# Kernel optimization log

Measured on AMD Instinct MI355X. Metric: run time of the kernel, lower is better.

## Reference

```python
import jax, jax.numpy as jnp
import numpy as np

H = 16   # n_heads == n_I
D = 64   # d_q = d_k = d_v = d_r
DX = H * D
B, S = 4, 2048

def setup_inputs() -> dict:
    key = jax.random.key(0)
    ks = jax.random.split(key, 9)
    sc = 0.02
    return {
        "value": jax.random.normal(ks[0], (B, S, DX), jnp.float32),
        "key":   jax.random.normal(ks[1], (B, S, DX), jnp.float32),
        "query": jax.random.normal(ks[2], (B, S, DX), jnp.float32),
        "Wq_w": jax.random.normal(ks[3], (DX, DX), jnp.float32) * sc,
        "Wq_b": jnp.zeros((DX,), jnp.float32),
        "Wk_w": jax.random.normal(ks[4], (DX, DX), jnp.float32) * sc,
        "Wk_b": jnp.zeros((DX,), jnp.float32),
        "Wv_w": jax.random.normal(ks[5], (DX, DX), jnp.float32) * sc,
        "Wv_b": jnp.zeros((DX,), jnp.float32),
        "Wr_w": jax.random.normal(ks[6], (DX, DX), jnp.float32) * sc,
        "Wr_b": jnp.zeros((DX,), jnp.float32),
        "Wout_w": jax.random.normal(ks[7], (DX, DX), jnp.float32) * sc,
        "Wout_b": jnp.zeros((DX,), jnp.float32),
    }

def _heads(x, b, s):
    # [b, s, H*D] -> [b, H, s, D]
    return x.reshape(b, s, H, D).transpose(0, 2, 1, 3)

def reference(value, key, query, Wq_w, Wq_b, Wk_w, Wk_b, Wv_w, Wv_b,
              Wr_w, Wr_b, Wout_w, Wout_b):
    b, s, _ = query.shape
    # torch nn.Linear: y = x @ W.T + b
    Q = _heads(query @ Wq_w.T + Wq_b, b, s)   # [b,H,s,D]
    K = _heads(key   @ Wk_w.T + Wk_b, b, s)
    V = _heads(value @ Wv_w.T + Wv_b, b, s)
    R = _heads(query @ Wr_w.T + Wr_b, b, s)
    dot_scale = jnp.sqrt(jnp.float32(D))
    scores = jnp.einsum("bhid,bhjd->bhij", Q, K) / dot_scale  # [b,H,s,s]
    attn = jax.nn.softmax(scores, axis=-1)                    # dropout p=0
    out = jnp.einsum("bhij,bhjd->bhid", attn, V)              # [b,H,s,D]
    out = out * R                                             # R-gating
    out = out.transpose(0, 2, 1, 3).reshape(b, s, H * D)
    return out @ Wout_w.T + Wout_b
```

## Files before the change

### kernel.cpp

```cpp
#include <hip/hip_runtime.h>
#include <hip/hip_bf16.h>

typedef __bf16 bf16;
typedef __bf16 bf16x4 __attribute__((ext_vector_type(4)));
typedef __bf16 bf16x8 __attribute__((ext_vector_type(8)));
typedef float  f32x4  __attribute__((ext_vector_type(4)));

#define MFMA_16x16x32(a, b, c) __builtin_amdgcn_mfma_f32_16x16x32_bf16((a), (b), (c), 0, 0, 0)

typedef const void __attribute__((address_space(1))) gvoid;
typedef void __attribute__((address_space(3))) svoid;

__device__ __forceinline__ void async_copy16(const void* gptr, void* ldsptr) {
    __builtin_amdgcn_global_load_lds((gvoid*)gptr, (svoid*)ldsptr, 16, 0, 0);
}

__device__ __forceinline__ int swz8(int row, int quad) {
    return (quad ^ ((row >> 1) & 3)) * 8;
}

__device__ __forceinline__ unsigned cvt_pk_bf16(float a, float b) {
    unsigned r;
    asm("v_cvt_pk_bf16_f32 %0, %1, %2" : "=v"(r) : "v"(a), "v"(b));
    return r;
}

__global__ void cvt3_acts(const float* __restrict__ s0, const float* __restrict__ s1,
                          const float* __restrict__ s2,
                          bf16* __restrict__ d0, bf16* __restrict__ d1, bf16* __restrict__ d2)
{
    constexpr int N4SEG = 8192 * 1024 / 4;
    int i = blockIdx.x * blockDim.x + threadIdx.x;
    const int stride = gridDim.x * blockDim.x;
    for (; i < 3 * N4SEG; i += stride) {
        const int seg = i / N4SEG;
        const int j = i - seg * N4SEG;
        const float* s = seg == 0 ? s0 : (seg == 1 ? s1 : s2);
        bf16* d = seg == 0 ? d0 : (seg == 1 ? d1 : d2);
        float4 v = ((const float4*)s)[j];
        bf16x4 o = { (bf16)v.x, (bf16)v.y, (bf16)v.z, (bf16)v.w };
        ((bf16x4*)d)[j] = o;
    }
}

__global__ void cvt5_wts(const float* __restrict__ s0, const float* __restrict__ s1,
                         const float* __restrict__ s2, const float* __restrict__ s3,
                         const float* __restrict__ s4,
                         bf16* __restrict__ d0, bf16* __restrict__ d1, bf16* __restrict__ d2,
                         bf16* __restrict__ d3, bf16* __restrict__ d4)
{
    constexpr int N4SEG = 1024 * 1024 / 4;
    int i = blockIdx.x * blockDim.x + threadIdx.x;
    const int stride = gridDim.x * blockDim.x;
    for (; i < 5 * N4SEG; i += stride) {
        const int seg = i / N4SEG;
        const int j = i - seg * N4SEG;
        const float* s = seg == 0 ? s0 : seg == 1 ? s1 : seg == 2 ? s2 : seg == 3 ? s3 : s4;
        bf16* d = seg == 0 ? d0 : seg == 1 ? d1 : seg == 2 ? d2 : seg == 3 ? d3 : d4;
        float4 v = ((const float4*)s)[j];
        bf16x4 o = { (bf16)v.x, (bf16)v.y, (bf16)v.z, (bf16)v.w };
        ((bf16x4*)d)[j] = o;
    }
}

__global__ void proj_fused(const bf16* __restrict__ xq, const bf16* __restrict__ xk,
                           const bf16* __restrict__ xv, const bf16* __restrict__ wall,
                           const float* __restrict__ ball,
                           bf16* __restrict__ qr, bf16* __restrict__ kws,
                           bf16* __restrict__ vtws)
{
    constexpr int K = 1024, SDIM = 2048;
    __shared__ alignas(16) bf16 As[2][128 * 32];
    __shared__ alignas(16) bf16 Bs[2][128 * 32];

    const int tid  = threadIdx.x;
    const int lane = tid & 63;
    const int wave = tid >> 6;
    const int wm   = wave >> 1;
    const int wn   = wave & 1;
    const int bm   = blockIdx.x * 128;
    const int by   = blockIdx.y;
    const int bn   = by * 128;
    const int l15  = lane & 15;
    const int quad = lane >> 4;

    const bf16* X = (by < 16) ? xq : (by < 24 ? xk : xv);

    const int srow = lane >> 2;
    const int scol = (lane & 3) * 8;

    const bf16* aseg0 = X + (size_t)(bm + wave * 32 + srow) * K + scol;
    const bf16* aseg1 = X + (size_t)(bm + wave * 32 + 16 + srow) * K + scol;
    const bf16* bseg0 = wall + (size_t)(bn + wave * 32 + srow) * K + scol;
    const bf16* bseg1 = wall + (size_t)(bn + wave * 32 + 16 + srow) * K + scol;

    f32x4 acc[4][4] = {};

    async_copy16(aseg0, As[0] + (wave * 2 + 0) * 512);
    async_copy16(aseg1, As[0] + (wave * 2 + 1) * 512);
    async_copy16(bseg0, Bs[0] + (wave * 2 + 0) * 512);
    async_copy16(bseg1, Bs[0] + (wave * 2 + 1) * 512);

    for (int k0 = 0; k0 < K; k0 += 32) {
        const int cur = (k0 >> 5) & 1;
        __syncthreads();
        if (k0 + 32 < K) {
            const int nxt = cur ^ 1;
            async_copy16(aseg0 + k0 + 32, As[nxt] + (wave * 2 + 0) * 512);
            async_copy16(aseg1 + k0 + 32, As[nxt] + (wave * 2 + 1) * 512);
            async_copy16(bseg0 + k0 + 32, Bs[nxt] + (wave * 2 + 0) * 512);
            async_copy16(bseg1 + k0 + 32, Bs[nxt] + (wave * 2 + 1) * 512);
        }

        bf16x8 af[4], bfr[4];
        #pragma unroll
        for (int i = 0; i < 4; ++i)
            af[i] = *(const bf16x8*)(As[cur] + (wm * 64 + i * 16 + l15) * 32 + quad * 8);
        #pragma unroll
        for (int j = 0; j < 4; ++j)
            bfr[j] = *(const bf16x8*)(Bs[cur] + (wn * 64 + j * 16 + l15) * 32 + quad * 8);
        #pragma unroll
        for (int i = 0; i < 4; ++i)
            #pragma unroll
            for (int j = 0; j < 4; ++j)
                acc[i][j] = MFMA_16x16x32(af[i], bfr[j], acc[i][j]);
    }

    #pragma unroll
    for (int i = 0; i < 4; ++i) {
        const int rowg = bm + wm * 64 + i * 16 + quad * 4;
        #pragma unroll
        for (int j = 0; j < 4; ++j) {
            const int colg = bn + wn * 64 + j * 16 + l15;
            const float bv = ball[colg];
            if (by < 16) {
                #pragma unroll
                for (int r = 0; r < 4; ++r)
                    qr[(size_t)(rowg + r) * 2048 + colg] = (bf16)(acc[i][j][r] + bv);
            } else if (by < 24) {
                const int cl = colg - 2048;
                #pragma unroll
                for (int r = 0; r < 4; ++r)
                    kws[(size_t)(rowg + r) * 1024 + cl] = (bf16)(acc[i][j][r] + bv);
            } else {
                const int d = colg - 3072;
                bf16x4 o;
                #pragma unroll
                for (int r = 0; r < 4; ++r) o[r] = (bf16)(acc[i][j][r] + bv);
                *(bf16x4*)(vtws + (size_t)(rowg >> 11) * 1024 * SDIM
                                + (size_t)d * SDIM + (rowg & (SDIM - 1))) = o;
            }
        }
    }
}

__global__ void gemm_out(const bf16* __restrict__ X, const bf16* __restrict__ W,
                         const float* __restrict__ bias, float* __restrict__ Y)
{
    constexpr int K = 1024, N = 1024;
    __shared__ alignas(16) bf16 As[2][128 * 32];
    __shared__ alignas(16) bf16 Bs[2][128 * 32];

    const int tid  = threadIdx.x;
    const int lane = tid & 63;
    const int wave = tid >> 6;
    const int wm   = wave >> 1;
    const int wn   = wave & 1;
    const int bm   = blockIdx.x * 128;
    const int bn   = blockIdx.y * 128;
    const int l15  = lane & 15;
    const int quad = lane >> 4;

    const int srow = lane >> 2;
    const int scol = (lane & 3) * 8;

    const bf16* aseg0 = X + (size_t)(bm + wave * 32 + srow) * K + scol;
    const bf16* aseg1 = X + (size_t)(bm + wave * 32 + 16 + srow) * K + scol;
    const bf16* bseg0 = W + (size_t)(bn + wave * 32 + srow) * K + scol;
    const bf16* bseg1 = W + (size_t)(bn + wave * 32 + 16 + srow) * K + scol;

    f32x4 acc[4][4] = {};

    async_copy16(aseg0, As[0] + (wave * 2 + 0) * 512);
    async_copy16(aseg1, As[0] + (wave * 2 + 1) * 512);
    async_copy16(bseg0, Bs[0] + (wave * 2 + 0) * 512);
    async_copy16(bseg1, Bs[0] + (wave * 2 + 1) * 512);

    for (int k0 = 0; k0 < K; k0 += 32) {
        const int cur = (k0 >> 5) & 1;
        __syncthreads();
        if (k0 + 32 < K) {
            const int nxt = cur ^ 1;
            async_copy16(aseg0 + k0 + 32, As[nxt] + (wave * 2 + 0) * 512);
            async_copy16(aseg1 + k0 + 32, As[nxt] + (wave * 2 + 1) * 512);
            async_copy16(bseg0 + k0 + 32, Bs[nxt] + (wave * 2 + 0) * 512);
            async_copy16(bseg1 + k0 + 32, Bs[nxt] + (wave * 2 + 1) * 512);
        }

        bf16x8 af[4], bfr[4];
        #pragma unroll
        for (int i = 0; i < 4; ++i)
            af[i] = *(const bf16x8*)(As[cur] + (wm * 64 + i * 16 + l15) * 32 + quad * 8);
        #pragma unroll
        for (int j = 0; j < 4; ++j)
            bfr[j] = *(const bf16x8*)(Bs[cur] + (wn * 64 + j * 16 + l15) * 32 + quad * 8);
        #pragma unroll
        for (int i = 0; i < 4; ++i)
            #pragma unroll
            for (int j = 0; j < 4; ++j)
                acc[i][j] = MFMA_16x16x32(af[i], bfr[j], acc[i][j]);
    }

    #pragma unroll
    for (int i = 0; i < 4; ++i) {
        const int rowg = bm + wm * 64 + i * 16 + quad * 4;
        #pragma unroll
        for (int j = 0; j < 4; ++j) {
            const int colg = bn + wn * 64 + j * 16 + l15;
            const float bv = bias[colg];
            #pragma unroll
            for (int r = 0; r < 4; ++r)
                Y[(size_t)(rowg + r) * N + colg] = acc[i][j][r] + bv;
        }
    }
}

__launch_bounds__(256, 2)
__global__ void attn_fused(const bf16* __restrict__ QRp, const bf16* __restrict__ Kp,
                           const bf16* __restrict__ Vtp, bf16* __restrict__ Op)
{
    constexpr int S = 2048, DXc = 1024, QRST = 2048, Dh = 64;
    constexpr int PST = 40;
    constexpr int NT = S / 64;
    __shared__ alignas(16) bf16 Ks[2][2][64 * 32];
    __shared__ alignas(16) bf16 Pt[4][2][2][16 * PST];

    const int tid  = threadIdx.x;
    const int lane = tid & 63;
    const int wave = tid >> 6;
    const int qt = blockIdx.x, h = blockIdx.y, b = blockIdx.z;
    const int l15  = lane & 15;
    const int quad = lane >> 4;

    const size_t qrbase = ((size_t)b * S) * QRST + h * Dh;
    const size_t kbase  = ((size_t)b * S) * DXc + h * Dh;
    const size_t vtbase = ((size_t)(b * 16 + h) * Dh) * S;
    const size_t obase  = ((size_t)b * S) * DXc + h * Dh;

    const int srow = lane >> 2;
    const int scol = ((lane & 3) ^ ((srow >> 1) & 3)) * 8;
    const bf16* kseg = Kp + kbase + (size_t)(16 * wave + srow) * DXc + scol;
    const int soff = wave * 512;

    const bf16* vwp = Vtp + vtbase + (size_t)l15 * S + quad * 8;

    async_copy16(kseg,      &Ks[0][0][soff]);
    async_copy16(kseg + 32, &Ks[0][1][soff]);

    constexpr float QSCALE = 0.125f * 1.44269504088896340736f;
    bf16x8 qf[2][2];
    #pragma unroll
    for (int mi = 0; mi < 2; ++mi) {
        const int qrow = qt * 128 + wave * 32 + mi * 16 + l15;
        const bf16* qptr = QRp + qrbase + (size_t)qrow * QRST + quad * 8;
        qf[mi][0] = *(const bf16x8*)(qptr);
        qf[mi][1] = *(const bf16x8*)(qptr + 32);
        #pragma unroll
        for (int j = 0; j < 8; ++j) {
            qf[mi][0][j] = (bf16)((float)qf[mi][0][j] * QSCALE);
            qf[mi][1][j] = (bf16)((float)qf[mi][1][j] * QSCALE);
        }
    }

    bf16x8 onef;
    #pragma unroll
    for (int j = 0; j < 8; ++j) onef[j] = (bf16)1.0f;

    f32x4 oacc[2][4] = {};
    f32x4 lsacc[2] = {};

    for (int t = 0; t < NT; ++t) {
        const int cur = t & 1;
        const int kv0 = t * 64;
        __syncthreads();
        if (t + 1 < NT) {
            const int nxt = cur ^ 1;
            const size_t ko = (size_t)(t + 1) * 64 * DXc;
            async_copy16(kseg + ko,      &Ks[nxt][0][soff]);
            async_copy16(kseg + ko + 32, &Ks[nxt][1][soff]);
        }

        bf16x8 vtf[2][4];
        #pragma unroll
        for (int half = 0; half < 2; ++half)
            #pragma unroll
            for (int db = 0; db < 4; ++db)
                vtf[half][db] = *(const bf16x8*)(vwp + (size_t)(db * 16) * S
                                                 + kv0 + half * 32);

        f32x4 st[2][4];
        #pragma unroll
        for (int nb = 0; nb < 4; ++nb) {
            bf16x8 kf0 = *(const bf16x8*)(&Ks[cur][0][0] + (nb * 16 + l15) * 32 + swz8(l15, quad));
            bf16x8 kf1 = *(const bf16x8*)(&Ks[cur][1][0] + (nb * 16 + l15) * 32 + swz8(l15, quad));
            #pragma unroll
            for (int mi = 0; mi < 2; ++mi) {
                f32x4 z = {0.f, 0.f, 0.f, 0.f};
                z = MFMA_16x16x32(kf1, qf[mi][1], z);
                st[mi][nb] = MFMA_16x16x32(kf0, qf[mi][0], z);
            }
        }
        #pragma unroll
        for (int mi = 0; mi < 2; ++mi) {
            #pragma unroll
            for (int nb = 0; nb < 4; ++nb) {
                const float p0 = __builtin_exp2f(st[mi][nb][0]);
                const float p1 = __builtin_exp2f(st[mi][nb][1]);
                const float p2 = __builtin_exp2f(st[mi][nb][2]);
                const float p3 = __builtin_exp2f(st[mi][nb][3]);
                uint2 w;
                w.x = cvt_pk_bf16(p0, p1);
                w.y = cvt_pk_bf16(p2, p3);
                *(uint2*)(&Pt[wave][mi][nb >> 1][0] + l15 * PST
                          + (nb & 1) * 16 + quad * 4) = w;
            }
        }
        #pragma unroll
        for (int half = 0; half < 2; ++half) {
            #pragma unroll
            for (int mi = 0; mi < 2; ++mi) {
                bf16x8 pf = *(const bf16x8*)(&Pt[wave][mi][half][0]
                                             + l15 * PST + quad * 8);
                #pragma unroll
                for (int db = 0; db < 4; ++db)
                    oacc[mi][db] = MFMA_16x16x32(vtf[half][db], pf, oacc[mi][db]);
                lsacc[mi] = MFMA_16x16x32(onef, pf, lsacc[mi]);
            }
        }
    }

    #pragma unroll
    for (int mi = 0; mi < 2; ++mi) {
        const float inv = 1.0f / lsacc[mi][0];
        const int qrow = qt * 128 + wave * 32 + mi * 16 + l15;
        const bf16* rrow = QRp + qrbase + (size_t)qrow * QRST + 1024;
        bf16* orow = Op + obase + (size_t)qrow * DXc;
        #pragma unroll
        for (int db = 0; db < 4; ++db) {
            bf16x4 rg = *(const bf16x4*)(rrow + db * 16 + quad * 4);
            bf16x4 o;
            #pragma unroll
            for (int r = 0; r < 4; ++r)
                o[r] = (bf16)(oacc[mi][db][r] * inv * (float)rg[r]);
            *(bf16x4*)(orow + db * 16 + quad * 4) = o;
        }
    }
}

extern "C" void kernel_launch(void* const* d_in, const int* in_sizes, int n_in,
                              void* d_out, int out_size, void* d_ws, size_t ws_size,
                              hipStream_t stream)
{
    (void)in_sizes; (void)n_in; (void)out_size; (void)ws_size;
    constexpr int B = 4, S = 2048, DX = 1024, M = B * S;
    constexpr size_t MD = (size_t)M * DX;
    constexpr size_t WD = (size_t)DX * DX;

    const float* value  = (const float*)d_in[0];
    const float* keyi   = (const float*)d_in[1];
    const float* query  = (const float*)d_in[2];
    const float* Wq_w   = (const float*)d_in[3];
    const float* Wq_b   = (const float*)d_in[4];
    const float* Wk_w   = (const float*)d_in[5];
    const float* Wk_b   = (const float*)d_in[6];
    const float* Wv_w   = (const float*)d_in[7];
    const float* Wv_b   = (const float*)d_in[8];
    const float* Wr_w   = (const float*)d_in[9];
    const float* Wr_b   = (const float*)d_in[10];
    const float* Wout_w = (const float*)d_in[11];
    const float* Wout_b = (const float*)d_in[12];

    bf16* p = (bf16*)d_ws;
    bf16* xv   = p;  p += MD;
    bf16* xk   = p;  p += MD;
    bf16* xq   = p;  p += MD;
    bf16* wall = p;  p += 4 * WD;
    bf16* wo   = p;  p += WD;
    bf16* qr   = p;  p += 2 * MD;
    bf16* kws  = p;  p += MD;
    bf16* vtws = p;  p += MD;
    float* ball = (float*)p;
    bf16* ows = xv;

    hipMemcpyAsync(ball,            Wq_b, DX * sizeof(float), hipMemcpyDeviceToDevice, stream);
    hipMemcpyAsync(ball + DX,       Wr_b, DX * sizeof(float), hipMemcpyDeviceToDevice, stream);
    hipMemcpyAsync(ball + 2 * DX,   Wk_b, DX * sizeof(float), hipMemcpyDeviceToDevice, stream);
    hipMemcpyAsync(ball + 3 * DX,   Wv_b, DX * sizeof(float), hipMemcpyDeviceToDevice, stream);

    cvt3_acts<<<dim3(2048), dim3(256), 0, stream>>>(value, keyi, query, xv, xk, xq);
    cvt5_wts <<<dim3(1024), dim3(256), 0, stream>>>(Wq_w, Wr_w, Wk_w, Wv_w, Wout_w,
                                                    wall, wall + WD, wall + 2 * WD,
                                                    wall + 3 * WD, wo);

    proj_fused<<<dim3(M / 128, 32), dim3(256), 0, stream>>>(
        xq, xk, xv, wall, ball, qr, kws, vtws);

    attn_fused<<<dim3(S / 128, 16, B), dim3(256), 0, stream>>>(qr, kws, vtws, ows);

    gemm_out<<<dim3(M / 128, DX / 128), dim3(256), 0, stream>>>(
        ows, wo, Wout_b, (float*)d_out);
}
```

Before: 480.5 us.

## Stage V tiles in LDS, remap GEMM workgroups, fold bias copies into weight conversion

The attention kernel now loads both K and V^T tiles into LDS through async copies each iteration, replacing V fragment loads straight from global memory. The K/V double buffering is dropped in favour of two barriers per tile. Occupancy is raised to 4 blocks per CU, and the grid is reordered so heads vary fastest. Both GEMMs get an XCD-aware workgroup remapping to improve L2 locality, and the four bias memcpys are folded into the weight-conversion kernel to save launches. Losing the prefetch overlap could expose K/V load latency, which the added occupancy is meant to hide.

```diff
diff --git a/kernel.cpp b/kernel.cpp
--- a/kernel.cpp
+++ b/kernel.cpp
@@ -46,12 +46,20 @@
 __global__ void cvt5_wts(const float* __restrict__ s0, const float* __restrict__ s1,
                          const float* __restrict__ s2, const float* __restrict__ s3,
                          const float* __restrict__ s4,
+                         const float* __restrict__ bq, const float* __restrict__ br,
+                         const float* __restrict__ bk, const float* __restrict__ bv,
                          bf16* __restrict__ d0, bf16* __restrict__ d1, bf16* __restrict__ d2,
-                         bf16* __restrict__ d3, bf16* __restrict__ d4)
+                         bf16* __restrict__ d3, bf16* __restrict__ d4,
+                         float* __restrict__ ball)
 {
     constexpr int N4SEG = 1024 * 1024 / 4;
     int i = blockIdx.x * blockDim.x + threadIdx.x;
     const int stride = gridDim.x * blockDim.x;
+    if (i < 4096) {
+        const int seg = i >> 10, j = i & 1023;
+        const float* b = seg == 0 ? bq : seg == 1 ? br : seg == 2 ? bk : bv;
+        ball[i] = b[j];
+    }
     for (; i < 5 * N4SEG; i += stride) {
         const int seg = i / N4SEG;
         const int j = i - seg * N4SEG;
@@ -73,13 +81,17 @@
     __shared__ alignas(16) bf16 As[2][128 * 32];
     __shared__ alignas(16) bf16 Bs[2][128 * 32];
 
+    const int lin  = blockIdx.x + 64 * blockIdx.y;
+    const int wgid = (lin & 7) * 256 + (lin >> 3);
+    const int bxr  = wgid & 63;
+    const int by   = wgid >> 6;
+
     const int tid  = threadIdx.x;
     const int lane = tid & 63;
     const int wave = tid >> 6;
     const int wm   = wave >> 1;
     const int wn   = wave & 1;
-    const int bm   = blockIdx.x * 128;
-    const int by   = blockIdx.y;
+    const int bm   = bxr * 128;
     const int bn   = by * 128;
     const int l15  = lane & 15;
     const int quad = lane >> 4;
@@ -161,13 +173,18 @@
     __shared__ alignas(16) bf16 As[2][128 * 32];
     __shared__ alignas(16) bf16 Bs[2][128 * 32];
 
+    const int lin  = blockIdx.x + 64 * blockIdx.y;
+    const int wgid = (lin & 7) * 64 + (lin >> 3);
+    const int bxr  = wgid & 63;
+    const int byr  = wgid >> 6;
+
     const int tid  = threadIdx.x;
     const int lane = tid & 63;
     const int wave = tid >> 6;
     const int wm   = wave >> 1;
     const int wn   = wave & 1;
-    const int bm   = blockIdx.x * 128;
-    const int bn   = blockIdx.y * 128;
+    const int bm   = bxr * 128;
+    const int bn   = byr * 128;
     const int l15  = lane & 15;
     const int quad = lane >> 4;
 
@@ -225,20 +242,20 @@
     }
 }
 
-__launch_bounds__(256, 2)
+__launch_bounds__(256, 4)
 __global__ void attn_fused(const bf16* __restrict__ QRp, const bf16* __restrict__ Kp,
                            const bf16* __restrict__ Vtp, bf16* __restrict__ Op)
 {
     constexpr int S = 2048, DXc = 1024, QRST = 2048, Dh = 64;
     constexpr int PST = 40;
-    constexpr int NT = S / 64;
-    __shared__ alignas(16) bf16 Ks[2][2][64 * 32];
+    __shared__ alignas(16) bf16 KsLo[64 * 32], KsHi[64 * 32];
+    __shared__ alignas(16) bf16 VtLo[64 * 32], VtHi[64 * 32];
     __shared__ alignas(16) bf16 Pt[4][2][2][16 * PST];
 
     const int tid  = threadIdx.x;
     const int lane = tid & 63;
     const int wave = tid >> 6;
-    const int qt = blockIdx.x, h = blockIdx.y, b = blockIdx.z;
+    const int h = blockIdx.x, qt = blockIdx.y, b = blockIdx.z;
     const int l15  = lane & 15;
     const int quad = lane >> 4;
 
@@ -246,16 +263,6 @@
     const size_t kbase  = ((size_t)b * S) * DXc + h * Dh;
     const size_t vtbase = ((size_t)(b * 16 + h) * Dh) * S;
     const size_t obase  = ((size_t)b * S) * DXc + h * Dh;
-
-    const int srow = lane >> 2;
-    const int scol = ((lane & 3) ^ ((srow >> 1) & 3)) * 8;
-    const bf16* kseg = Kp + kbase + (size_t)(16 * wave + srow) * DXc + scol;
-    const int soff = wave * 512;
-
-    const bf16* vwp = Vtp + vtbase + (size_t)l15 * S + quad * 8;
-
-    async_copy16(kseg,      &Ks[0][0][soff]);
-    async_copy16(kseg + 32, &Ks[0][1][soff]);
 
     constexpr float QSCALE = 0.125f * 1.44269504088896340736f;
     bf16x8 qf[2][2];
@@ -279,30 +286,28 @@
     f32x4 oacc[2][4] = {};
     f32x4 lsacc[2] = {};
 
-    for (int t = 0; t < NT; ++t) {
-        const int cur = t & 1;
-        const int kv0 = t * 64;
+    const int srow = lane >> 2;
+    const int scol = ((lane & 3) ^ ((srow >> 1) & 3)) * 8;
+    const bf16* kseg = Kp  + kbase  + (size_t)(16 * wave + srow) * DXc + scol;
+    const bf16* vseg = Vtp + vtbase + (size_t)(16 * wave + srow) * S   + scol;
+    bf16* ksl = KsLo + wave * 512;
+    bf16* ksh = KsHi + wave * 512;
+    bf16* vtl = VtLo + wave * 512;
+    bf16* vth = VtHi + wave * 512;
+
+    for (int kv0 = 0; kv0 < S; kv0 += 64) {
         __syncthreads();
-        if (t + 1 < NT) {
-            const int nxt = cur ^ 1;
-            const size_t ko = (size_t)(t + 1) * 64 * DXc;
-            async_copy16(kseg + ko,      &Ks[nxt][0][soff]);
-            async_copy16(kseg + ko + 32, &Ks[nxt][1][soff]);
-        }
-
-        bf16x8 vtf[2][4];
-        #pragma unroll
-        for (int half = 0; half < 2; ++half)
-            #pragma unroll
-            for (int db = 0; db < 4; ++db)
-                vtf[half][db] = *(const bf16x8*)(vwp + (size_t)(db * 16) * S
-                                                 + kv0 + half * 32);
+        async_copy16(kseg + (size_t)kv0 * DXc,      ksl);
+        async_copy16(kseg + (size_t)kv0 * DXc + 32, ksh);
+        async_copy16(vseg + kv0,                    vtl);
+        async_copy16(vseg + kv0 + 32,               vth);
+        __syncthreads();
 
         f32x4 st[2][4];
         #pragma unroll
         for (int nb = 0; nb < 4; ++nb) {
-            bf16x8 kf0 = *(const bf16x8*)(&Ks[cur][0][0] + (nb * 16 + l15) * 32 + swz8(l15, quad));
-            bf16x8 kf1 = *(const bf16x8*)(&Ks[cur][1][0] + (nb * 16 + l15) * 32 + swz8(l15, quad));
+            bf16x8 kf0 = *(const bf16x8*)(KsLo + (nb * 16 + l15) * 32 + swz8(l15, quad));
+            bf16x8 kf1 = *(const bf16x8*)(KsHi + (nb * 16 + l15) * 32 + swz8(l15, quad));
             #pragma unroll
             for (int mi = 0; mi < 2; ++mi) {
                 f32x4 z = {0.f, 0.f, 0.f, 0.f};
@@ -325,15 +330,21 @@
                           + (nb & 1) * 16 + quad * 4) = w;
             }
         }
+
         #pragma unroll
         for (int half = 0; half < 2; ++half) {
+            const bf16* vb = half ? VtHi : VtLo;
+            bf16x8 vtf[4];
+            #pragma unroll
+            for (int db = 0; db < 4; ++db)
+                vtf[db] = *(const bf16x8*)(vb + (db * 16 + l15) * 32 + swz8(l15, quad));
             #pragma unroll
             for (int mi = 0; mi < 2; ++mi) {
                 bf16x8 pf = *(const bf16x8*)(&Pt[wave][mi][half][0]
                                              + l15 * PST + quad * 8);
                 #pragma unroll
                 for (int db = 0; db < 4; ++db)
-                    oacc[mi][db] = MFMA_16x16x32(vtf[half][db], pf, oacc[mi][db]);
+                    oacc[mi][db] = MFMA_16x16x32(vtf[db], pf, oacc[mi][db]);
                 lsacc[mi] = MFMA_16x16x32(onef, pf, lsacc[mi]);
             }
         }
@@ -392,20 +403,16 @@
     float* ball = (float*)p;
     bf16* ows = xv;
 
-    hipMemcpyAsync(ball,            Wq_b, DX * sizeof(float), hipMemcpyDeviceToDevice, stream);
-    hipMemcpyAsync(ball + DX,       Wr_b, DX * sizeof(float), hipMemcpyDeviceToDevice, stream);
-    hipMemcpyAsync(ball + 2 * DX,   Wk_b, DX * sizeof(float), hipMemcpyDeviceToDevice, stream);
-    hipMemcpyAsync(ball + 3 * DX,   Wv_b, DX * sizeof(float), hipMemcpyDeviceToDevice, stream);
-
     cvt3_acts<<<dim3(2048), dim3(256), 0, stream>>>(value, keyi, query, xv, xk, xq);
     cvt5_wts <<<dim3(1024), dim3(256), 0, stream>>>(Wq_w, Wr_w, Wk_w, Wv_w, Wout_w,
+                                                    Wq_b, Wr_b, Wk_b, Wv_b,
                                                     wall, wall + WD, wall + 2 * WD,
-                                                    wall + 3 * WD, wo);
+                                                    wall + 3 * WD, wo, ball);
 
     proj_fused<<<dim3(M / 128, 32), dim3(256), 0, stream>>>(
         xq, xk, xv, wall, ball, qr, kws, vtws);
 
-    attn_fused<<<dim3(S / 128, 16, B), dim3(256), 0, stream>>>(qr, kws, vtws, ows);
+    attn_fused<<<dim3(16, S / 128, B), dim3(256), 0, stream>>>(qr, kws, vtws, ows);
 
     gemm_out<<<dim3(M / 128, DX / 128), dim3(256), 0, stream>>>(
         ows, wo, Wout_b, (float*)d_out);
```

Measured after the change: 401.7 us. 1.2x faster.
